# Kernel tuning notes

Measured on AMD Instinct MI355X. Metric: run time of the kernel, lower is better.

The kernel has to match this reference:

```python
import jax, jax.numpy as jnp
import numpy as np

NODE_DIM, HIDDEN, PROJ = 5, 128, 256
NUM_MP = 3
BOX = 1.0


def _knn_edges(positions, k, box_length=BOX):
    """Periodic kNN graph. positions: (B,N,3) -> (src, dst) global flat indices, E = B*N*k."""
    B, N, _ = positions.shape

    def per_batch(pos):  # (N,3)
        delta = jnp.abs(pos[:, None, :] - pos[None, :, :])          # (N,N,3)
        delta = jnp.where(delta > 0.5 * box_length, box_length - delta, delta)
        dist = jnp.sqrt(jnp.sum(delta * delta, axis=-1) + 1e-12)    # (N,N)
        _, idx = jax.lax.top_k(-dist, k + 1)                        # k+1 smallest
        return idx[:, 1:]                                           # drop self -> (N,k)

    nbrs = jax.vmap(per_batch)(positions)                           # (B,N,k)
    offset = (jnp.arange(B) * N)[:, None, None]
    src = jnp.broadcast_to(jnp.arange(N)[None, :, None], (B, N, k)) + offset
    dst = nbrs + offset
    return src.reshape(-1), dst.reshape(-1)


def setup_inputs() -> dict:
    key = jax.random.key(0)
    ks = jax.random.split(key, 16)
    B, N = 8, 2048
    s = 0.05
    inp = {
        "x": jax.random.normal(ks[0], (B, N, NODE_DIM), jnp.float32),
        "positions": jax.random.uniform(ks[1], (B, N, 3), jnp.float32),
        "k": 16,
        # encoder: Linear(5,128)+ReLU, Linear(128,128)+ReLU
        "enc_w0": jax.random.normal(ks[2], (NODE_DIM, HIDDEN), jnp.float32) * s,
        "enc_b0": jnp.zeros((HIDDEN,), jnp.float32),
        "enc_w1": jax.random.normal(ks[3], (HIDDEN, HIDDEN), jnp.float32) * s,
        "enc_b1": jnp.zeros((HIDDEN,), jnp.float32),
        # message nets: Linear(2H,H)+ReLU per round
        "msg_w": jax.random.normal(ks[4], (NUM_MP, 2 * HIDDEN, HIDDEN), jnp.float32) * s,
        "msg_b": jnp.zeros((NUM_MP, HIDDEN), jnp.float32),
        # update nets: Linear(2H,H)+ReLU per round
        "upd_w": jax.random.normal(ks[5], (NUM_MP, 2 * HIDDEN, HIDDEN), jnp.float32) * s,
        "upd_b": jnp.zeros((NUM_MP, HIDDEN), jnp.float32),
        # projection head: Linear(H,H)+ReLU, Linear(H,proj)
        "proj_w0": jax.random.normal(ks[6], (HIDDEN, HIDDEN), jnp.float32) * s,
        "proj_b0": jnp.zeros((HIDDEN,), jnp.float32),
        "proj_w1": jax.random.normal(ks[7], (HIDDEN, PROJ), jnp.float32) * s,
        "proj_b1": jnp.zeros((PROJ,), jnp.float32),
    }
    return inp


def reference(x, positions, k, enc_w0, enc_b0, enc_w1, enc_b1,
              msg_w, msg_b, upd_w, upd_b, proj_w0, proj_b0, proj_w1, proj_b1):
    B, N, _ = x.shape
    BN = B * N
    relu = jax.nn.relu

    # encoder over flattened nodes
    h = relu(x.reshape(BN, -1) @ enc_w0 + enc_b0)
    h = relu(h @ enc_w1 + enc_b1)

    src, dst = _knn_edges(positions, k)
    E = src.shape[0]
    deg = jax.ops.segment_sum(jnp.ones((E,), h.dtype), dst, num_segments=BN)
    inv_deg = 1.0 / jnp.clip(deg, 1.0)

    for i in range(NUM_MP):
        # per-edge message: concat(sender, receiver) -> Linear+ReLU
        msg = relu(jnp.concatenate([h[src], h[dst]], axis=-1) @ msg_w[i] + msg_b[i])
        # mean aggregation at destination nodes
        agg = jax.ops.segment_sum(msg, dst, num_segments=BN) * inv_deg[:, None]
        # residual update
        h = h + relu(jnp.concatenate([h, agg], axis=-1) @ upd_w[i] + upd_b[i])

    z = relu(h @ proj_w0 + proj_b0) @ proj_w1 + proj_b1
    return z.reshape(B, N, PROJ), h.reshape(B, N, HIDDEN)
```

## Files before the change

kernel.cpp:

```cpp
#include <hip/hip_runtime.h>
#include <stdint.h>
#include <math.h>

#define NN 2048
#define BB 8
#define BN (BB*NN)
#define KK 16
#define EE (BN*KK)
#define HID 128
#define PROJ_D 256
#define QPB 16
#define CDIM 6
#define NCELL (CDIM*CDIM*CDIM)
#define CAP 768

typedef unsigned long long u64;
typedef unsigned short ushort_t;
typedef __attribute__((ext_vector_type(8))) short short8;
typedef __attribute__((ext_vector_type(4))) float f32x4;

__device__ __forceinline__ u64 wave_min_u64(u64 v) {
  #pragma unroll
  for (int off = 32; off > 0; off >>= 1) {
    u64 o = __shfl_xor(v, off);
    v = o < v ? o : v;
  }
  return v;
}

__global__ __launch_bounds__(256) void cellsort_kernel(
    const float* __restrict__ pos, float4* __restrict__ spos,
    int* __restrict__ cptr) {
  __shared__ int hist[NCELL];
  __shared__ int base[NCELL];
  const int b = blockIdx.x, tid = threadIdx.x;
  if (tid < NCELL) hist[tid] = 0;
  __syncthreads();
  int cellv[8];
  float4 pv[8];
  #pragma unroll
  for (int k = 0; k < 8; k++) {
    int j = tid * 8 + k;
    const float* pp = pos + ((size_t)b * NN + j) * 3;
    float x = pp[0], y = pp[1], z = pp[2];
    int cx = (int)(x * 6.0f); cx = cx > 5 ? 5 : cx;
    int cy = (int)(y * 6.0f); cy = cy > 5 ? 5 : cy;
    int cz = (int)(z * 6.0f); cz = cz > 5 ? 5 : cz;
    int cell = (cx * 6 + cy) * 6 + cz;
    cellv[k] = cell;
    pv[k] = make_float4(x, y, z, __int_as_float(j));
    atomicAdd(&hist[cell], 1);
  }
  __syncthreads();
  if (tid == 0) {
    int run = 0;
    for (int c = 0; c < NCELL; c++) {
      cptr[b * (NCELL + 1) + c] = run;
      base[c] = run;
      run += hist[c];
    }
    cptr[b * (NCELL + 1) + NCELL] = run;
  }
  __syncthreads();
  if (tid < NCELL) hist[tid] = 0;
  __syncthreads();
  #pragma unroll
  for (int k = 0; k < 8; k++) {
    int slot = base[cellv[k]] + atomicAdd(&hist[cellv[k]], 1);
    spos[(size_t)b * NN + slot] = pv[k];
  }
}

__global__ __launch_bounds__(1024) void knn_kernel(
    const float4* __restrict__ spos, const int* __restrict__ cptr,
    int* __restrict__ nbr, int* __restrict__ cnt) {
  __shared__ float4 Ps[NN];
  __shared__ unsigned Hist[QPB * 256];
  __shared__ ushort_t Cand[QPB * CAP];
  __shared__ int Cp[NCELL + 1];
  const int b  = blockIdx.x >> 7;
  const int qb = blockIdx.x & 127;
  const int wave = threadIdx.x >> 6;
  const int lane = threadIdx.x & 63;
  const int s_q = qb * QPB + wave;

  for (int t = threadIdx.x; t < NN; t += 1024)
    Ps[t] = spos[(size_t)b * NN + t];
  if (threadIdx.x <= NCELL)
    Cp[threadIdx.x] = cptr[b * (NCELL + 1) + threadIdx.x];
  __syncthreads();

  const float4 q = Ps[s_q];
  const float xi = q.x, yi = q.y, zi = q.z;
  const int orig_i = __float_as_int(q.w);
  unsigned* H = &Hist[wave * 256];
  ushort_t* CL = &Cand[wave * CAP];

  int cx = (int)(xi * 6.0f); cx = cx > 5 ? 5 : cx;
  int cy = (int)(yi * 6.0f); cy = cy > 5 ? 5 : cy;
  int cz = (int)(zi * 6.0f); cz = cz > 5 ? 5 : cz;

  int T = 0;
  bool ovf = false;
  #pragma unroll 1
  for (int dxy = 0; dxy < 9; dxy++) {
    int dx = dxy / 3 - 1, dy = dxy - (dxy / 3) * 3 - 1;
    int ncx = cx + dx; ncx += (ncx < 0) ? 6 : 0; ncx -= (ncx >= 6) ? 6 : 0;
    int ncy = cy + dy; ncy += (ncy < 0) ? 6 : 0; ncy -= (ncy >= 6) ? 6 : 0;
    int cbse = (ncx * 6 + ncy) * 6;
    int s0, l0, s1 = 0, l1 = 0;
    if (cz == 0) {
      s0 = Cp[cbse + 5]; l0 = Cp[cbse + 6] - s0;
      s1 = Cp[cbse];     l1 = Cp[cbse + 2] - s1;
    } else if (cz == 5) {
      s0 = Cp[cbse + 4]; l0 = Cp[cbse + 6] - s0;
      s1 = Cp[cbse];     l1 = Cp[cbse + 1] - s1;
    } else {
      s0 = Cp[cbse + cz - 1]; l0 = Cp[cbse + cz + 2] - s0;
    }
    if (T + l0 + l1 > CAP) { ovf = true; break; }
    for (int t = lane; t < l0; t += 64) CL[T + t] = (ushort_t)(s0 + t);
    T += l0;
    for (int t = lane; t < l1; t += 64) CL[T + t] = (ushort_t)(s1 + t);
    T += l1;
  }

  int mode = ovf ? 1 : 0;
  float scale = 1536.0f;
  int T2 = T, binmax = 254;
  int bstar = 0; unsigned C = 0;
  for (;;) {
    scale = mode ? 256.0f : 1536.0f;
    T2 = mode ? NN : T;
    binmax = mode ? 256 : 254;
    *(uint4*)&H[lane * 4] = make_uint4(0u, 0u, 0u, 0u);
    for (int t = lane; t < T2; t += 64) {
      int p = mode ? t : (int)CL[t];
      float4 pj = Ps[p];
      float tx = xi - pj.x, ty = yi - pj.y, tz = zi - pj.z;
      float ddx = __fsub_rn(tx, rintf(tx));
      float ddy = __fsub_rn(ty, rintf(ty));
      float ddz = __fsub_rn(tz, rintf(tz));
      float s = __fadd_rn(__fadd_rn(__fadd_rn(__fmul_rn(ddx,ddx), __fmul_rn(ddy,ddy)),
                                    __fmul_rn(ddz,ddz)), 1e-12f);
      float d = __fsqrt_rn(s);
      int bin = (int)(d * scale);
      if (bin < binmax) atomicAdd(&H[bin], 1u);
    }
    uint4 cv = *(const uint4*)&H[lane * 4];
    unsigned s4 = cv.x + cv.y + cv.z + cv.w;
    unsigned incl = s4;
    #pragma unroll
    for (int off = 1; off < 64; off <<= 1) {
      unsigned v = __shfl_up(incl, off);
      if (lane >= off) incl += v;
    }
    unsigned total = __shfl(incl, 63);
    if (total >= 17u) {
      unsigned base = incl - s4;
      bool has = (incl >= 17u) && (base < 17u);
      u64 hmask = __ballot(has);
      int srcl = __ffsll((unsigned long long)hmask) - 1;
      int bl = 0; unsigned Cl = 0;
      if (has) {
        if (base + cv.x >= 17u)                    { bl = lane*4 + 0; Cl = base; }
        else if (base + cv.x + cv.y >= 17u)        { bl = lane*4 + 1; Cl = base + cv.x; }
        else if (base + cv.x + cv.y + cv.z >= 17u) { bl = lane*4 + 2; Cl = base + cv.x + cv.y; }
        else                                       { bl = lane*4 + 3; Cl = base + cv.x + cv.y + cv.z; }
      }
      bstar = __shfl(bl, srcl);
      C     = __shfl(Cl, srcl);
      break;
    }
    mode = 1;
  }
  const int m = 17 - (int)C;

  u64 lst[6];
  #pragma unroll
  for (int t = 0; t < 6; t++) lst[t] = ~0ull;
  for (int t = lane; t < T2; t += 64) {
    int p = mode ? t : (int)CL[t];
    float4 pj = Ps[p];
    float tx = xi - pj.x, ty = yi - pj.y, tz = zi - pj.z;
    float ddx = __fsub_rn(tx, rintf(tx));
    float ddy = __fsub_rn(ty, rintf(ty));
    float ddz = __fsub_rn(tz, rintf(tz));
    float s = __fadd_rn(__fadd_rn(__fadd_rn(__fmul_rn(ddx,ddx), __fmul_rn(ddy,ddy)),
                                  __fmul_rn(ddz,ddz)), 1e-12f);
    float d = __fsqrt_rn(s);
    int bin = (int)(d * scale);
    if (bin == bstar) {
      u64 key = ((u64)__float_as_uint(d) << 11) | (unsigned)__float_as_int(pj.w);
      if (key < lst[5]) {
        lst[5] = key;
        #pragma unroll
        for (int u = 5; u > 0; u--) {
          u64 a = lst[u-1], c2 = lst[u];
          lst[u-1] = a < c2 ? a : c2;
          lst[u]   = a < c2 ? c2 : a;
        }
      }
    }
  }

  u64 kstar = 0;
  #pragma unroll 1
  for (int r = 0; r < m; r++) {
    u64 h0 = lst[0];
    u64 gm = wave_min_u64(h0);
    kstar = gm;
    bool win = (h0 == gm);
    #pragma unroll
    for (int u = 0; u < 5; u++) lst[u] = win ? lst[u+1] : lst[u];
    lst[5] = win ? ~0ull : lst[5];
  }

  int* outp = nbr + ((size_t)b * NN + orig_i) * KK;
  int total_e = 0;
  for (int t0 = 0; t0 < T2; t0 += 64) {
    int t = t0 + lane;
    bool pred = false;
    int oj = 0;
    if (t < T2) {
      int p = mode ? t : (int)CL[t];
      float4 pj = Ps[p];
      float tx = xi - pj.x, ty = yi - pj.y, tz = zi - pj.z;
      float ddx = __fsub_rn(tx, rintf(tx));
      float ddy = __fsub_rn(ty, rintf(ty));
      float ddz = __fsub_rn(tz, rintf(tz));
      float s = __fadd_rn(__fadd_rn(__fadd_rn(__fmul_rn(ddx,ddx), __fmul_rn(ddy,ddy)),
                                    __fmul_rn(ddz,ddz)), 1e-12f);
      float d = __fsqrt_rn(s);
      oj = __float_as_int(pj.w);
      u64 key = ((u64)__float_as_uint(d) << 11) | (unsigned)oj;
      pred = (key <= kstar) && (oj != orig_i);
    }
    u64 msk = __ballot(pred);
    if (pred) {
      int ofs = total_e + __popcll(msk & ((1ull << lane) - 1ull));
      outp[ofs] = b * NN + oj;
      atomicAdd(&cnt[b * NN + oj], 1);
    }
    total_e += __popcll(msk);
  }
}

__global__ __launch_bounds__(256) void scan_kernel(const int* __restrict__ cnt,
                                                   int* __restrict__ row_ptr) {
  __shared__ int ps[256];
  int t = threadIdx.x;
  const int4* cv = (const int4*)(cnt + t * 64);
  int4 c[16];
  int s = 0;
  #pragma unroll
  for (int i = 0; i < 16; i++) {
    c[i] = cv[i];
    s += c[i].x + c[i].y + c[i].z + c[i].w;
  }
  ps[t] = s;
  __syncthreads();
  for (int off = 1; off < 256; off <<= 1) {
    int v = 0;
    if (t >= off) v = ps[t - off];
    __syncthreads();
    ps[t] += v;
    __syncthreads();
  }
  int run = t ? ps[t - 1] : 0;
  int4* rp = (int4*)(row_ptr + t * 64);
  #pragma unroll
  for (int i = 0; i < 16; i++) {
    int4 o;
    o.x = run; run += c[i].x;
    o.y = run; run += c[i].y;
    o.z = run; run += c[i].z;
    o.w = run; run += c[i].w;
    rp[i] = o;
  }
  if (t == 255) row_ptr[BN] = run;
}

__global__ __launch_bounds__(256) void fill_kernel(const int* __restrict__ nbr,
                                                   const int* __restrict__ row_ptr,
                                                   int* __restrict__ fill,
                                                   int* __restrict__ col) {
  int e = blockIdx.x * 256 + threadIdx.x;
  int d = nbr[e];
  int srcn = e >> 4;
  int p = row_ptr[d] + atomicAdd(&fill[d], 1);
  col[p] = srcn;
}

__global__ __launch_bounds__(256) void enc0_kernel(const float* __restrict__ x,
                                                   const float* __restrict__ w0,
                                                   const float* __restrict__ b0,
                                                   float* __restrict__ h) {
  int t = blockIdx.x * 256 + threadIdx.x;
  int m = t >> 5;
  int c = (t & 31) * 4;
  float xv[5];
  #pragma unroll
  for (int d = 0; d < 5; d++) xv[d] = x[m * 5 + d];
  float4 acc = *(const float4*)&b0[c];
  #pragma unroll
  for (int d = 0; d < 5; d++) {
    float4 w = *(const float4*)&w0[d * HID + c];
    acc.x += xv[d] * w.x; acc.y += xv[d] * w.y;
    acc.z += xv[d] * w.z; acc.w += xv[d] * w.w;
  }
  acc.x = fmaxf(acc.x, 0.f); acc.y = fmaxf(acc.y, 0.f);
  acc.z = fmaxf(acc.z, 0.f); acc.w = fmaxf(acc.w, 0.f);
  *(float4*)&h[(size_t)m * HID + c] = acc;
}

__device__ __forceinline__ unsigned cvtpk_bf16(float a, float b) {
  unsigned r;
  asm("v_cvt_pk_bf16_f32 %0, %1, %2" : "=v"(r) : "v"(a), "v"(b));
  return r;
}

__device__ __forceinline__ void cvt8(const float4 f0, const float4 f1,
                                     short8& hi, short8& lo) {
  unsigned h0 = cvtpk_bf16(f0.x, f0.y);
  unsigned h1 = cvtpk_bf16(f0.z, f0.w);
  unsigned h2 = cvtpk_bf16(f1.x, f1.y);
  unsigned h3 = cvtpk_bf16(f1.z, f1.w);
  unsigned l0 = cvtpk_bf16(f0.x - __uint_as_float(h0 << 16),
                           f0.y - __uint_as_float(h0 & 0xffff0000u));
  unsigned l1 = cvtpk_bf16(f0.z - __uint_as_float(h1 << 16),
                           f0.w - __uint_as_float(h1 & 0xffff0000u));
  unsigned l2 = cvtpk_bf16(f1.x - __uint_as_float(h2 << 16),
                           f1.y - __uint_as_float(h2 & 0xffff0000u));
  unsigned l3 = cvtpk_bf16(f1.z - __uint_as_float(h3 << 16),
                           f1.w - __uint_as_float(h3 & 0xffff0000u));
  union { unsigned u[4]; short8 v; } H, L;
  H.u[0] = h0; H.u[1] = h1; H.u[2] = h2; H.u[3] = h3;
  L.u[0] = l0; L.u[1] = l1; L.u[2] = l2; L.u[3] = l3;
  hi = H.v;
  lo = L.v;
}

__global__ __launch_bounds__(256) void prep_w_kernel(
    const float* __restrict__ enc_w1, const float* __restrict__ msg_w,
    const float* __restrict__ upd_w, const float* __restrict__ proj_w0,
    const float* __restrict__ proj_w1, ushort_t* __restrict__ wfrag) {
  int u = blockIdx.x >> 3;
  int c = (blockIdx.x & 7) * 256 + threadIdx.x;
  const float* src;
  int ldW = HID;
  if (u == 0) src = enc_w1;
  else if (u <= 6)  { int i = (u-1)>>1; int hf = (u-1)&1; src = msg_w + ((size_t)i*256 + hf*128) * HID; }
  else if (u <= 12) { int i = (u-7)>>1; int hf = (u-7)&1; src = upd_w + ((size_t)i*256 + hf*128) * HID; }
  else if (u == 13) src = proj_w0;
  else { src = proj_w1 + (u - 14) * 128; ldW = PROJ_D; }

  int ks = c >> 9, ct = (c >> 6) & 7, lane = c & 63;
  int colc = ct * 16 + (lane & 15);
  int k0 = ks * 32 + ((lane >> 4) << 3);
  float f[8];
  #pragma unroll
  for (int e = 0; e < 8; e++) f[e] = src[(size_t)(k0 + e) * ldW + colc];
  short8 hv, lv;
  cvt8(make_float4(f[0],f[1],f[2],f[3]), make_float4(f[4],f[5],f[6],f[7]), hv, lv);
  *(short8*)&wfrag[(size_t)u * 32768 + (size_t)c * 8] = hv;
  *(short8*)&wfrag[(size_t)u * 32768 + 16384 + (size_t)c * 8] = lv;
}

__device__ __forceinline__ void stage_A_convert(ushort_t* Ahi, ushort_t* Alo,
                                                const float* A, int m0, int tid) {
  #pragma unroll
  for (int i = 0; i < 4; i++) {
    int c = tid + i * 256;
    int row = c >> 4, kg = c & 15;
    const float4* ap = (const float4*)(A + (((size_t)m0 + row) << 7) + (kg << 3));
    short8 hv, lv;
    cvt8(ap[0], ap[1], hv, lv);
    int idx = (((row >> 4) * 4 + (kg >> 2)) * 64 + ((row & 15) | ((kg & 3) << 4))) * 8;
    *(short8*)&Ahi[idx] = hv;
    *(short8*)&Alo[idx] = lv;
  }
}

__device__ __forceinline__ void unit_mfma(f32x4 acc[8], const ushort_t* wf,
                                          const ushort_t* Ahi, const ushort_t* Alo,
                                          ushort_t* Bhi, ushort_t* Blo,
                                          int tid, int lane, int wid) {
  #pragma unroll 1
  for (int half = 0; half < 2; half++) {
    __syncthreads();
    const short8* ghi = (const short8*)(wf + half * 8192);
    const short8* glo = (const short8*)(wf + 16384 + half * 8192);
    #pragma unroll
    for (int i = 0; i < 4; i++) {
      ((short8*)Bhi)[tid + i * 256] = ghi[tid + i * 256];
      ((short8*)Blo)[tid + i * 256] = glo[tid + i * 256];
    }
    __syncthreads();
    #pragma unroll
    for (int ks2 = 0; ks2 < 2; ks2++) {
      int ksA = half * 2 + ks2;
      short8 ah = *(const short8*)&Ahi[((wid * 4 + ksA) * 64 + lane) * 8];
      short8 al = *(const short8*)&Alo[((wid * 4 + ksA) * 64 + lane) * 8];
      #pragma unroll
      for (int ct = 0; ct < 8; ct++) {
        short8 bh = *(const short8*)&Bhi[((ks2 * 8 + ct) * 64 + lane) * 8];
        short8 bl = *(const short8*)&Blo[((ks2 * 8 + ct) * 64 + lane) * 8];
        acc[ct] = __builtin_amdgcn_mfma_f32_16x16x32_bf16(ah, bh, acc[ct], 0, 0, 0);
        acc[ct] = __builtin_amdgcn_mfma_f32_16x16x32_bf16(ah, bl, acc[ct], 0, 0, 0);
        acc[ct] = __builtin_amdgcn_mfma_f32_16x16x32_bf16(al, bh, acc[ct], 0, 0, 0);
      }
    }
  }
}

__device__ __forceinline__ void unit_mfma_h(f32x4 acc[4], const ushort_t* wf,
                                            int ct0,
                                            const ushort_t* Ahi, const ushort_t* Alo,
                                            ushort_t* Bhi, ushort_t* Blo,
                                            int tid, int lane, int wid) {
  #pragma unroll 1
  for (int half = 0; half < 2; half++) {
    __syncthreads();
    #pragma unroll
    for (int i = 0; i < 2; i++) {
      int sc = tid + i * 256;
      int ks2 = sc >> 8;
      int cts = (sc >> 6) & 3;
      int ln  = sc & 63;
      int c = half * 1024 + ks2 * 512 + (ct0 + cts) * 64 + ln;
      ((short8*)Bhi)[sc] = *(const short8*)&wf[(size_t)c * 8];
      ((short8*)Blo)[sc] = *(const short8*)&wf[16384 + (size_t)c * 8];
    }
    __syncthreads();
    #pragma unroll
    for (int ks2 = 0; ks2 < 2; ks2++) {
      int ksA = half * 2 + ks2;
      short8 ah = *(const short8*)&Ahi[((wid * 4 + ksA) * 64 + lane) * 8];
      short8 al = *(const short8*)&Alo[((wid * 4 + ksA) * 64 + lane) * 8];
      #pragma unroll
      for (int ct = 0; ct < 4; ct++) {
        short8 bh = *(const short8*)&Bhi[((ks2 * 4 + ct) * 64 + lane) * 8];
        short8 bl = *(const short8*)&Blo[((ks2 * 4 + ct) * 64 + lane) * 8];
        acc[ct] = __builtin_amdgcn_mfma_f32_16x16x32_bf16(ah, bh, acc[ct], 0, 0, 0);
        acc[ct] = __builtin_amdgcn_mfma_f32_16x16x32_bf16(ah, bl, acc[ct], 0, 0, 0);
        acc[ct] = __builtin_amdgcn_mfma_f32_16x16x32_bf16(al, bh, acc[ct], 0, 0, 0);
      }
    }
  }
}

template<int RELU>
__global__ __launch_bounds__(256, 4) void g1_kernel(
    const float* __restrict__ A, const ushort_t* __restrict__ wf,
    const float* __restrict__ bias, float* __restrict__ out) {
  __shared__ ushort_t Ahi[8192], Alo[8192], Bhi[4096], Blo[4096];
  const int tid = threadIdx.x, lane = tid & 63, wid = tid >> 6;
  const int m0 = blockIdx.x * 64, ct0 = blockIdx.y * 4;
  stage_A_convert(Ahi, Alo, A, m0, tid);
  f32x4 acc[4];
  f32x4 z = {0.f, 0.f, 0.f, 0.f};
  #pragma unroll
  for (int ct = 0; ct < 4; ct++) acc[ct] = z;
  unit_mfma_h(acc, wf, ct0, Ahi, Alo, Bhi, Blo, tid, lane, wid);

  const int rbase = m0 + wid * 16 + ((lane >> 4) << 2);
  const int cb = lane & 15;
  #pragma unroll
  for (int ct = 0; ct < 4; ct++) {
    int n = (ct0 + ct) * 16 + cb;
    float bv = bias ? bias[n] : 0.f;
    #pragma unroll
    for (int r = 0; r < 4; r++) {
      float v = acc[ct][r] + bv;
      if (RELU) v = fmaxf(v, 0.f);
      out[(size_t)(rbase + r) * HID + n] = v;
    }
  }
}

__global__ __launch_bounds__(256, 4) void msg_kernel(
    const float* __restrict__ h, const ushort_t* __restrict__ wfT,
    const ushort_t* __restrict__ wfB, const float* __restrict__ mb,
    float* __restrict__ bufA, float* __restrict__ bufB) {
  __shared__ ushort_t Ahi[8192], Alo[8192], Bhi[8192], Blo[8192];
  const int tid = threadIdx.x, lane = tid & 63, wid = tid >> 6;
  const int m0 = blockIdx.x * 64;
  const int y = blockIdx.y;
  stage_A_convert(Ahi, Alo, h, m0, tid);
  f32x4 acc[8];
  f32x4 z = {0.f, 0.f, 0.f, 0.f};
  #pragma unroll
  for (int ct = 0; ct < 8; ct++) acc[ct] = z;
  unit_mfma(acc, y ? wfB : wfT, Ahi, Alo, Bhi, Blo, tid, lane, wid);

  float* out = y ? bufB : bufA;
  const float* bias = y ? mb : nullptr;
  const int rbase = m0 + wid * 16 + ((lane >> 4) << 2);
  const int cb = lane & 15;
  #pragma unroll
  for (int ct = 0; ct < 8; ct++) {
    int n = ct * 16 + cb;
    float bv = bias ? bias[n] : 0.f;
    #pragma unroll
    for (int r = 0; r < 4; r++)
      out[(size_t)(rbase + r) * HID + n] = acc[ct][r] + bv;
  }
}

__global__ __launch_bounds__(256, 4) void upd_kernel(
    const float* __restrict__ h, const ushort_t* __restrict__ wuT,
    const float* __restrict__ aggF, const ushort_t* __restrict__ wuB,
    const float* __restrict__ ub, float* __restrict__ out) {
  __shared__ ushort_t Ahi[8192], Alo[8192], Bhi[4096], Blo[4096];
  const int tid = threadIdx.x, lane = tid & 63, wid = tid >> 6;
  const int m0 = blockIdx.x * 64, ct0 = blockIdx.y * 4;
  stage_A_convert(Ahi, Alo, h, m0, tid);
  f32x4 acc[4];
  f32x4 z = {0.f, 0.f, 0.f, 0.f};
  #pragma unroll
  for (int ct = 0; ct < 4; ct++) acc[ct] = z;
  unit_mfma_h(acc, wuT, ct0, Ahi, Alo, Bhi, Blo, tid, lane, wid);
  __syncthreads();
  stage_A_convert(Ahi, Alo, aggF, m0, tid);
  unit_mfma_h(acc, wuB, ct0, Ahi, Alo, Bhi, Blo, tid, lane, wid);

  const int rbase = m0 + wid * 16 + ((lane >> 4) << 2);
  const int cb = lane & 15;
  #pragma unroll
  for (int ct = 0; ct < 4; ct++) {
    int n = (ct0 + ct) * 16 + cb;
    float bv = ub[n];
    #pragma unroll
    for (int r = 0; r < 4; r++) {
      float v = fmaxf(acc[ct][r] + bv, 0.f)
              + h[(size_t)(rbase + r) * HID + n];
      out[(size_t)(rbase + r) * HID + n] = v;
    }
  }
}

__global__ __launch_bounds__(256, 4) void proj1_kernel(
    const float* __restrict__ A, const ushort_t* __restrict__ wf01,
    const float* __restrict__ pb1, float* __restrict__ zout) {
  __shared__ ushort_t Ahi[8192], Alo[8192], Bhi[8192], Blo[8192];
  const int tid = threadIdx.x, lane = tid & 63, wid = tid >> 6;
  const int m0 = blockIdx.x * 64;
  const int y = blockIdx.y;
  stage_A_convert(Ahi, Alo, A, m0, tid);
  f32x4 acc[8];
  f32x4 z = {0.f, 0.f, 0.f, 0.f};
  #pragma unroll
  for (int ct = 0; ct < 8; ct++) acc[ct] = z;
  unit_mfma(acc, wf01 + (size_t)y * 32768, Ahi, Alo, Bhi, Blo, tid, lane, wid);

  const int rbase = m0 + wid * 16 + ((lane >> 4) << 2);
  const int cb = lane & 15;
  #pragma unroll
  for (int ct = 0; ct < 8; ct++) {
    int n = y * 128 + ct * 16 + cb;
    float bv = pb1[n];
    #pragma unroll
    for (int r = 0; r < 4; r++)
      zout[(size_t)(rbase + r) * PROJ_D + n] = acc[ct][r] + bv;
  }
}

__global__ __launch_bounds__(256) void agg_kernel(const float* __restrict__ Abuf,
                                                  const float* __restrict__ Bbuf,
                                                  const int* __restrict__ row_ptr,
                                                  const int* __restrict__ col,
                                                  float* __restrict__ agg) {
  int j = blockIdx.x * 2 + (threadIdx.x >> 7);
  int c = threadIdx.x & 127;
  float bj = Bbuf[(size_t)j * HID + c];
  int s = row_ptr[j], e = row_ptr[j + 1];
  float acc = 0.f;
  int p = s;
  for (; p + 4 <= e; p += 4) {
    int i0 = col[p], i1 = col[p+1], i2 = col[p+2], i3 = col[p+3];
    float v0 = Abuf[(size_t)i0 * HID + c];
    float v1 = Abuf[(size_t)i1 * HID + c];
    float v2 = Abuf[(size_t)i2 * HID + c];
    float v3 = Abuf[(size_t)i3 * HID + c];
    acc += fmaxf(v0 + bj, 0.f) + fmaxf(v1 + bj, 0.f)
         + fmaxf(v2 + bj, 0.f) + fmaxf(v3 + bj, 0.f);
  }
  for (; p < e; p++) {
    int i = col[p];
    acc += fmaxf(Abuf[(size_t)i * HID + c] + bj, 0.f);
  }
  float deg = (float)(e - s);
  float inv = 1.0f / fmaxf(deg, 1.0f);
  agg[(size_t)j * HID + c] = acc * inv;
}

extern "C" void kernel_launch(void* const* d_in, const int* in_sizes, int n_in,
                              void* d_out, int out_size, void* d_ws, size_t ws_size,
                              hipStream_t stream) {
  (void)in_sizes; (void)n_in; (void)out_size; (void)ws_size;
  const float* x       = (const float*)d_in[0];
  const float* pos     = (const float*)d_in[1];
  const float* enc_w0  = (const float*)d_in[3];
  const float* enc_b0  = (const float*)d_in[4];
  const float* enc_w1  = (const float*)d_in[5];
  const float* enc_b1  = (const float*)d_in[6];
  const float* msg_w   = (const float*)d_in[7];
  const float* msg_b   = (const float*)d_in[8];
  const float* upd_w   = (const float*)d_in[9];
  const float* upd_b   = (const float*)d_in[10];
  const float* proj_w0 = (const float*)d_in[11];
  const float* proj_b0 = (const float*)d_in[12];
  const float* proj_w1 = (const float*)d_in[13];
  const float* proj_b1 = (const float*)d_in[14];

  char* ws = (char*)d_ws;
  size_t off = 0;
  auto alloc = [&](size_t bytes) -> void* {
    void* p = ws + off;
    off += (bytes + 255) & ~(size_t)255;
    return p;
  };
  int*      nbr     = (int*)alloc((size_t)EE * 4);
  int*      cnt     = (int*)alloc((size_t)BN * 4);
  int*      fill    = (int*)alloc((size_t)BN * 4);
  int*      row_ptr = (int*)alloc((size_t)(BN + 1) * 4);
  int*      col     = (int*)alloc((size_t)EE * 4);
  float*    h_a     = (float*)alloc((size_t)BN * HID * 4);
  float*    h_b     = (float*)alloc((size_t)BN * HID * 4);
  float*    bufA    = (float*)alloc((size_t)BN * HID * 4);
  float*    bufB    = (float*)alloc((size_t)BN * HID * 4);
  float*    bufAgg  = (float*)alloc((size_t)BN * HID * 4);
  ushort_t* wfrag   = (ushort_t*)alloc((size_t)16 * 32768 * 2);
  float4*   spos    = (float4*)alloc((size_t)BN * 16);
  int*      cptr    = (int*)alloc((size_t)BB * (NCELL + 1) * 4);
  float*    out     = (float*)d_out;
  float*    hOut    = out + (size_t)BN * PROJ_D;

  hipMemsetAsync(cnt, 0, (size_t)BN * 4 * 2, stream);

  cellsort_kernel<<<BB, 256, 0, stream>>>(pos, spos, cptr);
  prep_w_kernel<<<128, 256, 0, stream>>>(enc_w1, msg_w, upd_w, proj_w0, proj_w1, wfrag);
  knn_kernel<<<BN / QPB, 1024, 0, stream>>>(spos, cptr, nbr, cnt);
  scan_kernel<<<1, 256, 0, stream>>>(cnt, row_ptr);
  fill_kernel<<<EE / 256, 256, 0, stream>>>(nbr, row_ptr, fill, col);

  enc0_kernel<<<BN * 32 / 256, 256, 0, stream>>>(x, enc_w0, enc_b0, bufA);
  g1_kernel<1><<<dim3(BN / 64, 2), 256, 0, stream>>>(bufA, wfrag + 0 * 32768,
                                                     enc_b1, h_a);

  float* hc = h_a;
  float* hn = h_b;
  for (int i = 0; i < 3; i++) {
    msg_kernel<<<dim3(BN / 64, 2), 256, 0, stream>>>(
        hc, wfrag + (size_t)(1 + 2 * i) * 32768,
        wfrag + (size_t)(2 + 2 * i) * 32768, msg_b + (size_t)i * HID,
        bufA, bufB);
    agg_kernel<<<BN / 2, 256, 0, stream>>>(bufA, bufB, row_ptr, col, bufAgg);
    float* target = (i == 2) ? hOut : hn;
    upd_kernel<<<dim3(BN / 64, 2), 256, 0, stream>>>(
        hc, wfrag + (size_t)(7 + 2 * i) * 32768, bufAgg,
        wfrag + (size_t)(8 + 2 * i) * 32768, upd_b + (size_t)i * HID, target);
    hn = hc; hc = target;
  }

  g1_kernel<1><<<dim3(BN / 64, 2), 256, 0, stream>>>(hc, wfrag + 13 * 32768,
                                                     proj_b0, bufA);
  proj1_kernel<<<dim3(BN / 64, 2), 256, 0, stream>>>(
      bufA, wfrag + 14 * 32768, proj_b1, out);
}
```

Before: 229.0 us.

## Fuse encoder layers, store message partials in bf16, fold memset into cellsort

```diff
diff --git a/kernel.cpp b/kernel.cpp
--- a/kernel.cpp
+++ b/kernel.cpp
@@ -30,10 +30,13 @@
 
 __global__ __launch_bounds__(256) void cellsort_kernel(
     const float* __restrict__ pos, float4* __restrict__ spos,
-    int* __restrict__ cptr) {
+    int* __restrict__ cptr, int4* __restrict__ cntz) {
   __shared__ int hist[NCELL];
   __shared__ int base[NCELL];
   const int b = blockIdx.x, tid = threadIdx.x;
+  #pragma unroll
+  for (int k = 0; k < 4; k++)
+    cntz[(b * 256 + tid) + k * 2048] = make_int4(0, 0, 0, 0);
   if (tid < NCELL) hist[tid] = 0;
   __syncthreads();
   int cellv[8];
@@ -292,28 +295,14 @@
   col[p] = srcn;
 }
 
-__global__ __launch_bounds__(256) void enc0_kernel(const float* __restrict__ x,
-                                                   const float* __restrict__ w0,
-                                                   const float* __restrict__ b0,
-                                                   float* __restrict__ h) {
-  int t = blockIdx.x * 256 + threadIdx.x;
-  int m = t >> 5;
-  int c = (t & 31) * 4;
-  float xv[5];
-  #pragma unroll
-  for (int d = 0; d < 5; d++) xv[d] = x[m * 5 + d];
-  float4 acc = *(const float4*)&b0[c];
-  #pragma unroll
-  for (int d = 0; d < 5; d++) {
-    float4 w = *(const float4*)&w0[d * HID + c];
-    acc.x += xv[d] * w.x; acc.y += xv[d] * w.y;
-    acc.z += xv[d] * w.z; acc.w += xv[d] * w.w;
-  }
-  acc.x = fmaxf(acc.x, 0.f); acc.y = fmaxf(acc.y, 0.f);
-  acc.z = fmaxf(acc.z, 0.f); acc.w = fmaxf(acc.w, 0.f);
-  *(float4*)&h[(size_t)m * HID + c] = acc;
-}
-
+__device__ __forceinline__ ushort_t bf16_rne(float x) {
+  unsigned u = __float_as_uint(x);
+  unsigned r = u + 0x7FFFu + ((u >> 16) & 1u);
+  return (ushort_t)(r >> 16);
+}
+__device__ __forceinline__ float bf16_to_f(ushort_t h) {
+  return __uint_as_float(((unsigned)h) << 16);
+}
 __device__ __forceinline__ unsigned cvtpk_bf16(float a, float b) {
   unsigned r;
   asm("v_cvt_pk_bf16_f32 %0, %1, %2" : "=v"(r) : "v"(a), "v"(b));
@@ -450,6 +439,65 @@
   }
 }
 
+__global__ __launch_bounds__(256, 4) void encg1_kernel(
+    const float* __restrict__ x, const float* __restrict__ ew0,
+    const float* __restrict__ eb0, const ushort_t* __restrict__ wf,
+    const float* __restrict__ eb1, float* __restrict__ hOut) {
+  __shared__ ushort_t Ahi[8192], Alo[8192], Bhi[4096], Blo[4096];
+  __shared__ float XW[1088];
+  const int tid = threadIdx.x, lane = tid & 63, wid = tid >> 6;
+  const int m0 = blockIdx.x * 64, ct0 = blockIdx.y * 4;
+
+  if (tid < 80) ((float4*)XW)[tid] = ((const float4*)(x + (size_t)m0 * 5))[tid];
+  else if (tid < 240) ((float4*)XW)[tid] = ((const float4*)ew0)[tid - 80];
+  else {
+    int k = tid - 240;
+    ((float4*)XW)[240 + k] = ((const float4*)eb0)[k];
+    ((float4*)XW)[256 + k] = ((const float4*)eb0)[16 + k];
+  }
+  __syncthreads();
+
+  #pragma unroll
+  for (int i = 0; i < 4; i++) {
+    int c = tid + i * 256;
+    int row = c >> 4, kg = c & 15;
+    float xr[5];
+    #pragma unroll
+    for (int d = 0; d < 5; d++) xr[d] = XW[row * 5 + d];
+    float v[8];
+    #pragma unroll
+    for (int e = 0; e < 8; e++) {
+      int col = kg * 8 + e;
+      float a = XW[960 + col];
+      #pragma unroll
+      for (int d = 0; d < 5; d++) a += xr[d] * XW[320 + d * 128 + col];
+      v[e] = fmaxf(a, 0.f);
+    }
+    short8 hv, lv;
+    cvt8(make_float4(v[0],v[1],v[2],v[3]), make_float4(v[4],v[5],v[6],v[7]), hv, lv);
+    int idx = (((row >> 4) * 4 + (kg >> 2)) * 64 + ((row & 15) | ((kg & 3) << 4))) * 8;
+    *(short8*)&Ahi[idx] = hv;
+    *(short8*)&Alo[idx] = lv;
+  }
+
+  f32x4 acc[4];
+  f32x4 z = {0.f, 0.f, 0.f, 0.f};
+  #pragma unroll
+  for (int ct = 0; ct < 4; ct++) acc[ct] = z;
+  unit_mfma_h(acc, wf, ct0, Ahi, Alo, Bhi, Blo, tid, lane, wid);
+
+  const int rbase = m0 + wid * 16 + ((lane >> 4) << 2);
+  const int cb = lane & 15;
+  #pragma unroll
+  for (int ct = 0; ct < 4; ct++) {
+    int n = (ct0 + ct) * 16 + cb;
+    float bv = eb1[n];
+    #pragma unroll
+    for (int r = 0; r < 4; r++)
+      hOut[(size_t)(rbase + r) * HID + n] = fmaxf(acc[ct][r] + bv, 0.f);
+  }
+}
+
 template<int RELU>
 __global__ __launch_bounds__(256, 4) void g1_kernel(
     const float* __restrict__ A, const ushort_t* __restrict__ wf,
@@ -482,7 +530,7 @@
 __global__ __launch_bounds__(256, 4) void msg_kernel(
     const float* __restrict__ h, const ushort_t* __restrict__ wfT,
     const ushort_t* __restrict__ wfB, const float* __restrict__ mb,
-    float* __restrict__ bufA, float* __restrict__ bufB) {
+    ushort_t* __restrict__ bufA, ushort_t* __restrict__ bufB) {
   __shared__ ushort_t Ahi[8192], Alo[8192], Bhi[8192], Blo[8192];
   const int tid = threadIdx.x, lane = tid & 63, wid = tid >> 6;
   const int m0 = blockIdx.x * 64;
@@ -494,7 +542,7 @@
   for (int ct = 0; ct < 8; ct++) acc[ct] = z;
   unit_mfma(acc, y ? wfB : wfT, Ahi, Alo, Bhi, Blo, tid, lane, wid);
 
-  float* out = y ? bufB : bufA;
+  ushort_t* out = y ? bufB : bufA;
   const float* bias = y ? mb : nullptr;
   const int rbase = m0 + wid * 16 + ((lane >> 4) << 2);
   const int cb = lane & 15;
@@ -504,7 +552,7 @@
     float bv = bias ? bias[n] : 0.f;
     #pragma unroll
     for (int r = 0; r < 4; r++)
-      out[(size_t)(rbase + r) * HID + n] = acc[ct][r] + bv;
+      out[(size_t)(rbase + r) * HID + n] = bf16_rne(acc[ct][r] + bv);
   }
 }
 
@@ -566,29 +614,29 @@
   }
 }
 
-__global__ __launch_bounds__(256) void agg_kernel(const float* __restrict__ Abuf,
-                                                  const float* __restrict__ Bbuf,
+__global__ __launch_bounds__(256) void agg_kernel(const ushort_t* __restrict__ Abuf,
+                                                  const ushort_t* __restrict__ Bbuf,
                                                   const int* __restrict__ row_ptr,
                                                   const int* __restrict__ col,
                                                   float* __restrict__ agg) {
   int j = blockIdx.x * 2 + (threadIdx.x >> 7);
   int c = threadIdx.x & 127;
-  float bj = Bbuf[(size_t)j * HID + c];
+  float bj = bf16_to_f(Bbuf[(size_t)j * HID + c]);
   int s = row_ptr[j], e = row_ptr[j + 1];
   float acc = 0.f;
   int p = s;
   for (; p + 4 <= e; p += 4) {
     int i0 = col[p], i1 = col[p+1], i2 = col[p+2], i3 = col[p+3];
-    float v0 = Abuf[(size_t)i0 * HID + c];
-    float v1 = Abuf[(size_t)i1 * HID + c];
-    float v2 = Abuf[(size_t)i2 * HID + c];
-    float v3 = Abuf[(size_t)i3 * HID + c];
+    float v0 = bf16_to_f(Abuf[(size_t)i0 * HID + c]);
+    float v1 = bf16_to_f(Abuf[(size_t)i1 * HID + c]);
+    float v2 = bf16_to_f(Abuf[(size_t)i2 * HID + c]);
+    float v3 = bf16_to_f(Abuf[(size_t)i3 * HID + c]);
     acc += fmaxf(v0 + bj, 0.f) + fmaxf(v1 + bj, 0.f)
          + fmaxf(v2 + bj, 0.f) + fmaxf(v3 + bj, 0.f);
   }
   for (; p < e; p++) {
     int i = col[p];
-    acc += fmaxf(Abuf[(size_t)i * HID + c] + bj, 0.f);
+    acc += fmaxf(bf16_to_f(Abuf[(size_t)i * HID + c]) + bj, 0.f);
   }
   float deg = (float)(e - s);
   float inv = 1.0f / fmaxf(deg, 1.0f);
@@ -628,8 +676,8 @@
   int*      col     = (int*)alloc((size_t)EE * 4);
   float*    h_a     = (float*)alloc((size_t)BN * HID * 4);
   float*    h_b     = (float*)alloc((size_t)BN * HID * 4);
-  float*    bufA    = (float*)alloc((size_t)BN * HID * 4);
-  float*    bufB    = (float*)alloc((size_t)BN * HID * 4);
+  ushort_t* bufA    = (ushort_t*)alloc((size_t)BN * HID * 2);
+  ushort_t* bufB    = (ushort_t*)alloc((size_t)BN * HID * 2);
   float*    bufAgg  = (float*)alloc((size_t)BN * HID * 4);
   ushort_t* wfrag   = (ushort_t*)alloc((size_t)16 * 32768 * 2);
   float4*   spos    = (float4*)alloc((size_t)BN * 16);
@@ -637,17 +685,14 @@
   float*    out     = (float*)d_out;
   float*    hOut    = out + (size_t)BN * PROJ_D;
 
-  hipMemsetAsync(cnt, 0, (size_t)BN * 4 * 2, stream);
-
-  cellsort_kernel<<<BB, 256, 0, stream>>>(pos, spos, cptr);
+  cellsort_kernel<<<BB, 256, 0, stream>>>(pos, spos, cptr, (int4*)cnt);
   prep_w_kernel<<<128, 256, 0, stream>>>(enc_w1, msg_w, upd_w, proj_w0, proj_w1, wfrag);
   knn_kernel<<<BN / QPB, 1024, 0, stream>>>(spos, cptr, nbr, cnt);
   scan_kernel<<<1, 256, 0, stream>>>(cnt, row_ptr);
   fill_kernel<<<EE / 256, 256, 0, stream>>>(nbr, row_ptr, fill, col);
 
-  enc0_kernel<<<BN * 32 / 256, 256, 0, stream>>>(x, enc_w0, enc_b0, bufA);
-  g1_kernel<1><<<dim3(BN / 64, 2), 256, 0, stream>>>(bufA, wfrag + 0 * 32768,
-                                                     enc_b1, h_a);
+  encg1_kernel<<<dim3(BN / 64, 2), 256, 0, stream>>>(
+      x, enc_w0, enc_b0, wfrag + 0 * 32768, enc_b1, h_a);
 
   float* hc = h_a;
   float* hn = h_b;
@@ -665,7 +710,7 @@
   }
 
   g1_kernel<1><<<dim3(BN / 64, 2), 256, 0, stream>>>(hc, wfrag + 13 * 32768,
-                                                     proj_b0, bufA);
+                                                     proj_b0, h_b);
   proj1_kernel<<<dim3(BN / 64, 2), 256, 0, stream>>>(
-      bufA, wfrag + 14 * 32768, proj_b1, out);
-}
+      h_b, wfrag + 14 * 32768, proj_b1, out);
+}
```

Measured after the change: 214.1 us. 6.5% less time.
